# Kernel tuning notes

Measured on AMD Instinct MI355X. Metric: run time of the kernel, lower is better.

The kernel has to match this reference:

```python
import jax, jax.numpy as jnp
import numpy as np

N_NODES = 50000
N_EDGES = 800000
DIM = 128
BN_EPS = 1e-5


def setup_inputs() -> dict:
    key = jax.random.key(0)
    k1, k2, k3 = jax.random.split(key, 3)
    x = jax.random.normal(k1, (N_NODES, DIM), dtype=jnp.float32)
    edge_index = jax.random.randint(k2, (2, N_EDGES), 0, N_NODES, dtype=jnp.int64)
    W = jax.random.normal(k3, (DIM, DIM), dtype=jnp.float32) / np.sqrt(DIM)
    b = jnp.zeros((DIM,), dtype=jnp.float32)
    gamma = jnp.ones((DIM,), dtype=jnp.float32)
    beta = jnp.zeros((DIM,), dtype=jnp.float32)
    return {"x": x, "edge_index": edge_index, "W": W, "b": b,
            "gamma": gamma, "beta": beta}


def reference(x, edge_index, W, b, gamma, beta):
    # GCNConv(flow='target_to_source') with add_self_loops=True, edge_weight=None.
    N = x.shape[0]
    # add self loops with weight 1
    loops = jnp.tile(jnp.arange(N, dtype=edge_index.dtype)[None, :], (2, 1))
    ei = jnp.concatenate([edge_index, loops], axis=1)  # [2, E+N]
    row, col = ei[0], ei[1]
    ew = jnp.ones(ei.shape[1], dtype=x.dtype)
    # gcn_norm: for flow != 'source_to_target', degree is computed on row index
    deg = jax.ops.segment_sum(ew, row, num_segments=N)
    dinv = jnp.where(deg > 0, deg ** -0.5, 0.0)
    norm = dinv[row] * ew * dinv[col]  # [E+N]
    xw = x @ W  # [N, D] linear transform (no bias inside, bias added after agg)
    # flow='target_to_source': message from col (target), aggregate at row (source)
    msg = xw[col] * norm[:, None]      # [E+N, D] gather + scale
    out = jax.ops.segment_sum(msg, row, num_segments=N) + b  # scatter-add
    # BatchNorm1d (training-mode batch statistics)
    mean = out.mean(axis=0)
    var = out.var(axis=0)
    y = (out - mean) * jax.lax.rsqrt(var + BN_EPS) * gamma + beta
    # ReLU + residual
    return jax.nn.relu(y) + x
```

## Files before the change

### kernel.cpp

```cpp
#include <hip/hip_runtime.h>

#define DIM 128
#define BN_EPS 1e-5f
#define CAP 64

typedef __attribute__((ext_vector_type(8))) short short8;
typedef __attribute__((ext_vector_type(4))) float f32x4;

static __host__ size_t align256(size_t x) { return (x + 255) & ~(size_t)255; }

__device__ __forceinline__ unsigned short f2bf(float f) {
    unsigned int u = __float_as_uint(f);
    unsigned int r = (u + 0x7fffu + ((u >> 16) & 1u)) >> 16;
    return (unsigned short)r;
}

__global__ __launch_bounds__(256) void k_prep(const float* __restrict__ W,
                                              unsigned short* __restrict__ Wt,
                                              int* __restrict__ cursor,
                                              float* __restrict__ stats, int N) {
    int t = blockIdx.x * 256 + threadIdx.x;
    if (t < DIM * DIM) {
        int n = t >> 7, k = t & 127;
        Wt[t] = f2bf(W[k * DIM + n]);
    }
    if (t < N) cursor[t] = t << 6;
    if (t < 256) stats[t] = 0.f;
}

__global__ __launch_bounds__(256) void k_gemm_fill(const float* __restrict__ x,
                                                   const unsigned short* __restrict__ Wt,
                                                   const int* __restrict__ ei,
                                                   int* __restrict__ cursor,
                                                   int* __restrict__ bucket,
                                                   unsigned short* __restrict__ xw,
                                                   int N, int E, int Gg) {
    const int tid = threadIdx.x;
    if (blockIdx.x >= Gg) {
        const int f = blockIdx.x - Gg;
        const int part = f & 7;
        const int bi = f >> 3;
        const int nb = (gridDim.x - Gg) >> 3;
        const int S = nb * 256;
        const int psz = (N + 7) >> 3;
        const int lo = part * psz;
        const int hi = (lo + psz < N) ? lo + psz : N;
        int e = bi * 256 + tid;
        for (; e + 3 * S < E; e += 4 * S) {
            int r[4];
            #pragma unroll
            for (int j = 0; j < 4; ++j) r[j] = ei[e + j * S];
            int pos[4];
            bool in[4];
            #pragma unroll
            for (int j = 0; j < 4; ++j) {
                in[j] = (r[j] >= lo) & (r[j] < hi);
                if (in[j]) pos[j] = atomicAdd(&cursor[r[j]], 1);
            }
            #pragma unroll
            for (int j = 0; j < 4; ++j)
                if (in[j] && pos[j] < (r[j] << 6) + CAP) bucket[pos[j]] = ei[E + e + j * S];
        }
        for (; e < E; e += S) {
            int r = ei[e];
            if (r >= lo && r < hi) {
                int pos = atomicAdd(&cursor[r], 1);
                if (pos < (r << 6) + CAP) bucket[pos] = ei[E + e];
            }
        }
        return;
    }

    const int w = tid >> 6;
    const int lane = tid & 63;
    const int quad = lane >> 4;
    const int l15 = lane & 15;
    const int rbase = (blockIdx.x * 4 + w) * 32;
    if (rbase >= N) return;

    short8 a[2][4];
    #pragma unroll
    for (int s = 0; s < 2; ++s) {
        const int row = rbase + s * 16 + l15;
        #pragma unroll
        for (int kk = 0; kk < 4; ++kk) {
            short8 frag;
            if (row < N) {
                const float4* p = (const float4*)(x + (size_t)row * DIM + kk * 32 + quad * 8);
                float4 v0 = p[0], v1 = p[1];
                frag[0] = (short)f2bf(v0.x); frag[1] = (short)f2bf(v0.y);
                frag[2] = (short)f2bf(v0.z); frag[3] = (short)f2bf(v0.w);
                frag[4] = (short)f2bf(v1.x); frag[5] = (short)f2bf(v1.y);
                frag[6] = (short)f2bf(v1.z); frag[7] = (short)f2bf(v1.w);
            } else {
                frag = (short8)0;
            }
            a[s][kk] = frag;
        }
    }

    #pragma unroll
    for (int ct = 0; ct < 8; ++ct) {
        short8 bfr[4];
        #pragma unroll
        for (int kk = 0; kk < 4; ++kk)
            bfr[kk] = *(const short8*)(Wt + (ct * 16 + l15) * DIM + kk * 32 + quad * 8);
        f32x4 acc0 = {0.f, 0.f, 0.f, 0.f}, acc1 = {0.f, 0.f, 0.f, 0.f};
        #pragma unroll
        for (int kk = 0; kk < 4; ++kk) {
            acc0 = __builtin_amdgcn_mfma_f32_16x16x32_bf16(a[0][kk], bfr[kk], acc0, 0, 0, 0);
            acc1 = __builtin_amdgcn_mfma_f32_16x16x32_bf16(a[1][kk], bfr[kk], acc1, 0, 0, 0);
        }
        const int col = ct * 16 + l15;
        #pragma unroll
        for (int r = 0; r < 4; ++r) {
            int g0 = rbase + quad * 4 + r;
            if (g0 < N) xw[(size_t)g0 * DIM + col] = f2bf(acc0[r]);
            int g1 = g0 + 16;
            if (g1 < N) xw[(size_t)g1 * DIM + col] = f2bf(acc1[r]);
        }
    }
}

__device__ __forceinline__ float dinv_of(const int* cursor, int c) {
    return rsqrtf((float)(cursor[c] - (c << 6) + 1));
}

__global__ __launch_bounds__(256) void k_agg(const unsigned int* __restrict__ xw_u32,
                                             const int* __restrict__ cursor,
                                             const int* __restrict__ bucket,
                                             const float* __restrict__ b,
                                             float* __restrict__ stats,
                                             float* __restrict__ out, int N) {
    const int wid = threadIdx.x >> 6;
    const int lane = threadIdx.x & 63;
    const int wstride = gridDim.x * 4;
    float s1x = 0.f, s1y = 0.f, s2x = 0.f, s2y = 0.f;
    const float2 bb = ((const float2*)b)[lane];

    for (int node = blockIdx.x * 4 + wid; node < N; node += wstride) {
        const int start = node << 6;
        int cnt = cursor[node] - start;
        const float di = rsqrtf((float)(cnt + 1));
        if (cnt > CAP) cnt = CAP;
        unsigned int u = xw_u32[(size_t)node * 64 + lane];
        float ax = di * __uint_as_float(u << 16);
        float ay = di * __uint_as_float(u & 0xffff0000u);
        const int epos = start + cnt;
        int e = start;
        for (; e + 7 < epos; e += 8) {
            int c[8];
            #pragma unroll
            for (int j = 0; j < 8; ++j) c[j] = bucket[e + j];
            float dc[8];
            unsigned int uu[8];
            #pragma unroll
            for (int j = 0; j < 8; ++j) {
                dc[j] = dinv_of(cursor, c[j]);
                uu[j] = xw_u32[(size_t)c[j] * 64 + lane];
            }
            #pragma unroll
            for (int j = 0; j < 8; ++j) {
                ax = fmaf(dc[j], __uint_as_float(uu[j] << 16), ax);
                ay = fmaf(dc[j], __uint_as_float(uu[j] & 0xffff0000u), ay);
            }
        }
        for (; e + 1 < epos; e += 2) {
            int c0 = bucket[e], c1 = bucket[e + 1];
            float d0 = dinv_of(cursor, c0), d1 = dinv_of(cursor, c1);
            unsigned int u0 = xw_u32[(size_t)c0 * 64 + lane];
            unsigned int u1 = xw_u32[(size_t)c1 * 64 + lane];
            ax = fmaf(d0, __uint_as_float(u0 << 16), ax);
            ay = fmaf(d0, __uint_as_float(u0 & 0xffff0000u), ay);
            ax = fmaf(d1, __uint_as_float(u1 << 16), ax);
            ay = fmaf(d1, __uint_as_float(u1 & 0xffff0000u), ay);
        }
        if (e < epos) {
            int c0 = bucket[e];
            float d0 = dinv_of(cursor, c0);
            unsigned int u0 = xw_u32[(size_t)c0 * 64 + lane];
            ax = fmaf(d0, __uint_as_float(u0 << 16), ax);
            ay = fmaf(d0, __uint_as_float(u0 & 0xffff0000u), ay);
        }
        float ox = bb.x + di * ax;
        float oy = bb.y + di * ay;
        ((float2*)out)[(size_t)node * 64 + lane] = make_float2(ox, oy);
        s1x += ox; s2x += ox * ox;
        s1y += oy; s2y += oy * oy;
    }

    __shared__ float4 red[256];
    red[threadIdx.x] = make_float4(s1x, s1y, s2x, s2y);
    __syncthreads();
    if (threadIdx.x < 64) {
        float4 a0 = red[threadIdx.x];
        float4 a1 = red[64 + threadIdx.x];
        float4 a2 = red[128 + threadIdx.x];
        float4 a3 = red[192 + threadIdx.x];
        float v1x = a0.x + a1.x + a2.x + a3.x;
        float v1y = a0.y + a1.y + a2.y + a3.y;
        float v2x = a0.z + a1.z + a2.z + a3.z;
        float v2y = a0.w + a1.w + a2.w + a3.w;
        int l = threadIdx.x;
        atomicAdd(&stats[2 * l], v1x);
        atomicAdd(&stats[2 * l + 1], v1y);
        atomicAdd(&stats[128 + 2 * l], v2x);
        atomicAdd(&stats[128 + 2 * l + 1], v2y);
    }
}

__global__ void k_final(const float* __restrict__ x, const float* __restrict__ stats,
                        const float* __restrict__ gamma, const float* __restrict__ beta,
                        float* __restrict__ out, int total, float invN) {
    int gid = blockIdx.x * blockDim.x + threadIdx.x;
    if (gid >= total) return;
    int d = gid & 127;
    float mean = stats[d] * invN;
    float var = stats[128 + d] * invN - mean * mean;
    float y = (out[gid] - mean) * rsqrtf(var + BN_EPS) * gamma[d] + beta[d];
    out[gid] = fmaxf(y, 0.f) + x[gid];
}

extern "C" void kernel_launch(void* const* d_in, const int* in_sizes, int n_in,
                              void* d_out, int out_size, void* d_ws, size_t ws_size,
                              hipStream_t stream) {
    const float* x     = (const float*)d_in[0];
    const int*   ei    = (const int*)d_in[1];
    const float* W     = (const float*)d_in[2];
    const float* b     = (const float*)d_in[3];
    const float* gamma = (const float*)d_in[4];
    const float* beta  = (const float*)d_in[5];
    float* out = (float*)d_out;

    const int N = in_sizes[0] / DIM;
    const int E = in_sizes[1] / 2;
    const int total = N * DIM;
    const int Gg = (((N + 127) / 128) + 7) & ~7;
    const int Gf = 2048;

    char* ws = (char*)d_ws;
    size_t off = 0;
    float* stats = (float*)(ws + off);     off = align256(off + 1024);
    unsigned short* Wt = (unsigned short*)(ws + off); off = align256(off + (size_t)DIM * DIM * 2);
    int* cursor = (int*)(ws + off);        off = align256(off + (size_t)N * 4);
    int* bucket = (int*)(ws + off);        off = align256(off + (size_t)N * CAP * 4);
    unsigned short* xw = (unsigned short*)(ws + off);

    k_prep<<<(N + 255) / 256, 256, 0, stream>>>(W, Wt, cursor, stats, N);
    k_gemm_fill<<<Gg + Gf, 256, 0, stream>>>(x, Wt, ei, cursor, bucket, xw, N, E, Gg);
    k_agg<<<1024, 256, 0, stream>>>((const unsigned int*)xw, cursor, bucket, b, stats, out, N);
    k_final<<<(total + 255) / 256, 256, 0, stream>>>(x, stats, gamma, beta, out, total, 1.0f / N);
}
```

Measured before the change: 228.5 us.

## Split BN stats into separate kernel, one-wave-per-node agg grid, vectorize final

The aggregation kernel switches from a persistent grid-stride loop that also accumulated batch-norm statistics to a grid with one wavefront per node and no stats work. A new k_stats kernel re-reads the output to compute per-column sums and sums of squares. Bucket indices are now loaded as int4, and the final normalize/ReLU/residual kernel is vectorized to float4. This is meant to improve load balance and occupancy in the gather, but it adds an extra full read of the 25.6 MB output and one more kernel launch.

```diff
diff --git a/kernel.cpp b/kernel.cpp
--- a/kernel.cpp
+++ b/kernel.cpp
@@ -130,95 +130,108 @@
                                              const int* __restrict__ cursor,
                                              const int* __restrict__ bucket,
                                              const float* __restrict__ b,
-                                             float* __restrict__ stats,
                                              float* __restrict__ out, int N) {
-    const int wid = threadIdx.x >> 6;
+    const int node = blockIdx.x * 4 + (threadIdx.x >> 6);
+    if (node >= N) return;
     const int lane = threadIdx.x & 63;
-    const int wstride = gridDim.x * 4;
-    float s1x = 0.f, s1y = 0.f, s2x = 0.f, s2y = 0.f;
-    const float2 bb = ((const float2*)b)[lane];
-
-    for (int node = blockIdx.x * 4 + wid; node < N; node += wstride) {
-        const int start = node << 6;
-        int cnt = cursor[node] - start;
-        const float di = rsqrtf((float)(cnt + 1));
-        if (cnt > CAP) cnt = CAP;
-        unsigned int u = xw_u32[(size_t)node * 64 + lane];
-        float ax = di * __uint_as_float(u << 16);
-        float ay = di * __uint_as_float(u & 0xffff0000u);
-        const int epos = start + cnt;
-        int e = start;
-        for (; e + 7 < epos; e += 8) {
-            int c[8];
-            #pragma unroll
-            for (int j = 0; j < 8; ++j) c[j] = bucket[e + j];
-            float dc[8];
-            unsigned int uu[8];
-            #pragma unroll
-            for (int j = 0; j < 8; ++j) {
-                dc[j] = dinv_of(cursor, c[j]);
-                uu[j] = xw_u32[(size_t)c[j] * 64 + lane];
-            }
-            #pragma unroll
-            for (int j = 0; j < 8; ++j) {
-                ax = fmaf(dc[j], __uint_as_float(uu[j] << 16), ax);
-                ay = fmaf(dc[j], __uint_as_float(uu[j] & 0xffff0000u), ay);
-            }
-        }
-        for (; e + 1 < epos; e += 2) {
-            int c0 = bucket[e], c1 = bucket[e + 1];
-            float d0 = dinv_of(cursor, c0), d1 = dinv_of(cursor, c1);
-            unsigned int u0 = xw_u32[(size_t)c0 * 64 + lane];
-            unsigned int u1 = xw_u32[(size_t)c1 * 64 + lane];
-            ax = fmaf(d0, __uint_as_float(u0 << 16), ax);
-            ay = fmaf(d0, __uint_as_float(u0 & 0xffff0000u), ay);
-            ax = fmaf(d1, __uint_as_float(u1 << 16), ax);
-            ay = fmaf(d1, __uint_as_float(u1 & 0xffff0000u), ay);
-        }
-        if (e < epos) {
-            int c0 = bucket[e];
-            float d0 = dinv_of(cursor, c0);
-            unsigned int u0 = xw_u32[(size_t)c0 * 64 + lane];
-            ax = fmaf(d0, __uint_as_float(u0 << 16), ax);
-            ay = fmaf(d0, __uint_as_float(u0 & 0xffff0000u), ay);
-        }
-        float ox = bb.x + di * ax;
-        float oy = bb.y + di * ay;
-        ((float2*)out)[(size_t)node * 64 + lane] = make_float2(ox, oy);
-        s1x += ox; s2x += ox * ox;
-        s1y += oy; s2y += oy * oy;
-    }
-
-    __shared__ float4 red[256];
-    red[threadIdx.x] = make_float4(s1x, s1y, s2x, s2y);
+    const int start = node << 6;
+    int cnt = cursor[node] - start;
+    const float di = rsqrtf((float)(cnt + 1));
+    if (cnt > CAP) cnt = CAP;
+    unsigned int u = xw_u32[(size_t)node * 64 + lane];
+    float ax = di * __uint_as_float(u << 16);
+    float ay = di * __uint_as_float(u & 0xffff0000u);
+    const int epos = start + cnt;
+    int e = start;
+    for (; e + 7 < epos; e += 8) {
+        int4 q0 = *(const int4*)(bucket + e);
+        int4 q1 = *(const int4*)(bucket + e + 4);
+        int c[8] = {q0.x, q0.y, q0.z, q0.w, q1.x, q1.y, q1.z, q1.w};
+        float dc[8];
+        unsigned int uu[8];
+        #pragma unroll
+        for (int j = 0; j < 8; ++j) {
+            dc[j] = dinv_of(cursor, c[j]);
+            uu[j] = xw_u32[(size_t)c[j] * 64 + lane];
+        }
+        #pragma unroll
+        for (int j = 0; j < 8; ++j) {
+            ax = fmaf(dc[j], __uint_as_float(uu[j] << 16), ax);
+            ay = fmaf(dc[j], __uint_as_float(uu[j] & 0xffff0000u), ay);
+        }
+    }
+    for (; e + 1 < epos; e += 2) {
+        int c0 = bucket[e], c1 = bucket[e + 1];
+        float d0 = dinv_of(cursor, c0), d1 = dinv_of(cursor, c1);
+        unsigned int u0 = xw_u32[(size_t)c0 * 64 + lane];
+        unsigned int u1 = xw_u32[(size_t)c1 * 64 + lane];
+        ax = fmaf(d0, __uint_as_float(u0 << 16), ax);
+        ay = fmaf(d0, __uint_as_float(u0 & 0xffff0000u), ay);
+        ax = fmaf(d1, __uint_as_float(u1 << 16), ax);
+        ay = fmaf(d1, __uint_as_float(u1 & 0xffff0000u), ay);
+    }
+    if (e < epos) {
+        int c0 = bucket[e];
+        float d0 = dinv_of(cursor, c0);
+        unsigned int u0 = xw_u32[(size_t)c0 * 64 + lane];
+        ax = fmaf(d0, __uint_as_float(u0 << 16), ax);
+        ay = fmaf(d0, __uint_as_float(u0 & 0xffff0000u), ay);
+    }
+    float2 bb = ((const float2*)b)[lane];
+    float2 o;
+    o.x = bb.x + di * ax;
+    o.y = bb.y + di * ay;
+    ((float2*)out)[(size_t)node * 64 + lane] = o;
+}
+
+__global__ __launch_bounds__(256) void k_stats(const float4* __restrict__ out4,
+                                               float* __restrict__ stats, int n4) {
+    const int tid = threadIdx.x;
+    float4 s1 = make_float4(0.f, 0.f, 0.f, 0.f);
+    float4 s2 = make_float4(0.f, 0.f, 0.f, 0.f);
+    for (int i = blockIdx.x * 256 + tid; i < n4; i += gridDim.x * 256) {
+        float4 v = out4[i];
+        s1.x += v.x; s1.y += v.y; s1.z += v.z; s1.w += v.w;
+        s2.x += v.x * v.x; s2.y += v.y * v.y; s2.z += v.z * v.z; s2.w += v.w * v.w;
+    }
+    __shared__ float4 r1[256], r2[256];
+    r1[tid] = s1; r2[tid] = s2;
     __syncthreads();
-    if (threadIdx.x < 64) {
-        float4 a0 = red[threadIdx.x];
-        float4 a1 = red[64 + threadIdx.x];
-        float4 a2 = red[128 + threadIdx.x];
-        float4 a3 = red[192 + threadIdx.x];
-        float v1x = a0.x + a1.x + a2.x + a3.x;
-        float v1y = a0.y + a1.y + a2.y + a3.y;
-        float v2x = a0.z + a1.z + a2.z + a3.z;
-        float v2y = a0.w + a1.w + a2.w + a3.w;
-        int l = threadIdx.x;
-        atomicAdd(&stats[2 * l], v1x);
-        atomicAdd(&stats[2 * l + 1], v1y);
-        atomicAdd(&stats[128 + 2 * l], v2x);
-        atomicAdd(&stats[128 + 2 * l + 1], v2y);
-    }
-}
-
-__global__ void k_final(const float* __restrict__ x, const float* __restrict__ stats,
+    if (tid < 32) {
+        float4 a1 = r1[tid], a2 = r2[tid];
+        #pragma unroll
+        for (int k = 1; k < 8; ++k) {
+            float4 b1 = r1[tid + 32 * k], b2 = r2[tid + 32 * k];
+            a1.x += b1.x; a1.y += b1.y; a1.z += b1.z; a1.w += b1.w;
+            a2.x += b2.x; a2.y += b2.y; a2.z += b2.z; a2.w += b2.w;
+        }
+        const int d = tid * 4;
+        atomicAdd(&stats[d + 0], a1.x); atomicAdd(&stats[d + 1], a1.y);
+        atomicAdd(&stats[d + 2], a1.z); atomicAdd(&stats[d + 3], a1.w);
+        atomicAdd(&stats[128 + d + 0], a2.x); atomicAdd(&stats[128 + d + 1], a2.y);
+        atomicAdd(&stats[128 + d + 2], a2.z); atomicAdd(&stats[128 + d + 3], a2.w);
+    }
+}
+
+__global__ void k_final(const float4* __restrict__ x4, const float* __restrict__ stats,
                         const float* __restrict__ gamma, const float* __restrict__ beta,
-                        float* __restrict__ out, int total, float invN) {
-    int gid = blockIdx.x * blockDim.x + threadIdx.x;
-    if (gid >= total) return;
-    int d = gid & 127;
-    float mean = stats[d] * invN;
-    float var = stats[128 + d] * invN - mean * mean;
-    float y = (out[gid] - mean) * rsqrtf(var + BN_EPS) * gamma[d] + beta[d];
-    out[gid] = fmaxf(y, 0.f) + x[gid];
+                        float4* __restrict__ out4, int n4, float invN) {
+    int i = blockIdx.x * blockDim.x + threadIdx.x;
+    if (i >= n4) return;
+    const int d = (i & 31) * 4;
+    float4 o = out4[i];
+    float4 xr = x4[i];
+    float res[4];
+    float ov[4] = {o.x, o.y, o.z, o.w};
+    float xv[4] = {xr.x, xr.y, xr.z, xr.w};
+    #pragma unroll
+    for (int j = 0; j < 4; ++j) {
+        float mean = stats[d + j] * invN;
+        float var = stats[128 + d + j] * invN - mean * mean;
+        float y = (ov[j] - mean) * rsqrtf(var + BN_EPS) * gamma[d + j] + beta[d + j];
+        res[j] = fmaxf(y, 0.f) + xv[j];
+    }
+    out4[i] = make_float4(res[0], res[1], res[2], res[3]);
 }
 
 extern "C" void kernel_launch(void* const* d_in, const int* in_sizes, int n_in,
@@ -235,6 +248,7 @@
     const int N = in_sizes[0] / DIM;
     const int E = in_sizes[1] / 2;
     const int total = N * DIM;
+    const int n4 = total / 4;
     const int Gg = (((N + 127) / 128) + 7) & ~7;
     const int Gf = 2048;
 
@@ -248,6 +262,8 @@
 
     k_prep<<<(N + 255) / 256, 256, 0, stream>>>(W, Wt, cursor, stats, N);
     k_gemm_fill<<<Gg + Gf, 256, 0, stream>>>(x, Wt, ei, cursor, bucket, xw, N, E, Gg);
-    k_agg<<<1024, 256, 0, stream>>>((const unsigned int*)xw, cursor, bucket, b, stats, out, N);
-    k_final<<<(total + 255) / 256, 256, 0, stream>>>(x, stats, gamma, beta, out, total, 1.0f / N);
-}
+    k_agg<<<(N + 3) / 4, 256, 0, stream>>>((const unsigned int*)xw, cursor, bucket, b, out, N);
+    k_stats<<<1024, 256, 0, stream>>>((const float4*)out, stats, n4);
+    k_final<<<(n4 + 255) / 256, 256, 0, stream>>>((const float4*)x, stats, gamma, beta,
+                                                  (float4*)out, n4, 1.0f / N);
+}
```

Measured after the change: 275.9 us. 20.8% more time.
